# Kernel optimization log

Hardware: AMD Instinct MI355X
Metric: run time of the kernel (lower is better)

The kernel has to match this reference:

```python
import jax, jax.numpy as jnp
import numpy as np

B, IMG, TXT, N, FF, HID, C, E = 1024, 512, 300, 14, 2048, 128, 14, 182
D = IMG + TXT  # 812, transformer d_model


def setup_inputs() -> dict:
    key = jax.random.key(0)
    ks = jax.random.split(key, 12)
    r = lambda k, s, sc=0.02: (jax.random.normal(k, s, jnp.float32) * sc)
    return {
        "img_feat": jax.random.normal(ks[0], (B, IMG), jnp.float32),
        "word_embeds": jax.random.normal(ks[1], (N, TXT), jnp.float32),
        "edge_index": jax.random.randint(ks[2], (2, E), 0, N, jnp.int32),
        "in_proj_w": r(ks[3], (3 * D, D)),
        "in_proj_b": jnp.zeros((3 * D,), jnp.float32),
        "out_proj_w": r(ks[4], (D, D)),
        "out_proj_b": jnp.zeros((D,), jnp.float32),
        "ln1_g": jnp.ones((D,), jnp.float32), "ln1_b": jnp.zeros((D,), jnp.float32),
        "ln2_g": jnp.ones((D,), jnp.float32), "ln2_b": jnp.zeros((D,), jnp.float32),
        "ffn_w1": r(ks[5], (D, FF)), "ffn_b1": jnp.zeros((FF,), jnp.float32),
        "ffn_w2": r(ks[6], (FF, D)), "ffn_b2": jnp.zeros((D,), jnp.float32),
        "gcn1_w": r(ks[7], (D, HID)), "gcn1_b": jnp.zeros((HID,), jnp.float32),
        "gcn2_w": r(ks[8], (HID, HID)), "gcn2_b": jnp.zeros((HID,), jnp.float32),
        "lin_w": r(ks[9], (HID, C)), "lin_b": jnp.zeros((C,), jnp.float32),
    }


def layer_norm(x, g, b, eps=1e-5):
    mu = x.mean(-1, keepdims=True)
    var = ((x - mu) ** 2).mean(-1, keepdims=True)
    return (x - mu) * jax.lax.rsqrt(var + eps) * g + b


def gcn_conv(x, edge_index, W, b, n_nodes):
    # PyG GCNConv: add self loops, symmetric normalization, x @ W then scatter-add.
    # x: (B, N, F_in); gather/scatter along node axis (node_dim=-2).
    src, dst = edge_index[0], edge_index[1]
    loop = jnp.arange(n_nodes, dtype=src.dtype)
    src = jnp.concatenate([src, loop])
    dst = jnp.concatenate([dst, loop])
    deg = jnp.zeros((n_nodes,), x.dtype).at[dst].add(1.0)
    dinv = jnp.where(deg > 0, deg ** -0.5, 0.0)
    ew = dinv[src] * dinv[dst]                       # (E+N,)
    h = x @ W                                        # (B, N, F_out)
    msg = h[:, src, :] * ew[None, :, None]           # gather neighbors
    out = jnp.zeros_like(h).at[:, dst, :].add(msg)   # scatter-aggregate
    return out + b


def reference(img_feat, word_embeds, edge_index,
              in_proj_w, in_proj_b, out_proj_w, out_proj_b,
              ln1_g, ln1_b, ln2_g, ln2_b,
              ffn_w1, ffn_b1, ffn_w2, ffn_b2,
              gcn1_w, gcn1_b, gcn2_w, gcn2_b, lin_w, lin_b):
    # Broadcast image feature across the 14 label nodes; concat word embeddings.
    node = jnp.concatenate([
        jnp.broadcast_to(img_feat[:, None, :], (B, N, IMG)),
        jnp.broadcast_to(word_embeds[None, :, :], (B, N, TXT)),
    ], axis=-1)                                      # (B, N, D)

    # torch TransformerEncoderLayer, batch_first=False, nhead=1, post-norm, relu.
    # Input (B, N, D) is interpreted as (seq=B, batch=N, D): attention over dim 0.
    qkv = node @ in_proj_w.T + in_proj_b
    q, k, v = jnp.split(qkv, 3, axis=-1)             # each (B, N, D)
    scale = 1.0 / jnp.sqrt(jnp.asarray(D, node.dtype))
    scores = jnp.einsum('lnd,mnd->nlm', q, k) * scale  # (N, B, B)
    attn = jax.nn.softmax(scores, axis=-1)
    ao = jnp.einsum('nlm,mnd->lnd', attn, v)           # (B, N, D)
    ao = ao @ out_proj_w.T + out_proj_b
    x = layer_norm(node + ao, ln1_g, ln1_b)
    ff = jax.nn.relu(x @ ffn_w1 + ffn_b1) @ ffn_w2 + ffn_b2
    x = layer_norm(x + ff, ln2_g, ln2_b)               # (B, N, D)

    # Two GCNConv layers over the 14-node label graph (batched over B).
    x = jax.nn.relu(gcn_conv(x, edge_index, gcn1_w, gcn1_b, N))
    x = gcn_conv(x, edge_index, gcn2_w, gcn2_b, N)
    x = jax.nn.relu(x.mean(axis=1))                    # mean over nodes -> (B, HID)
    return x @ lin_w + lin_b                           # (B, C)
```

## Files before the change

### kernel.cpp

```cpp
#include <hip/hip_runtime.h>
#include <math.h>

#define B_    1024
#define IMG_  512
#define TXT_  300
#define NN_   14
#define FF_   2048
#define HID_  128
#define CC_   14
#define EE_   182
#define DD_   812
#define D3_   2436
#define BNR_  14336
#define KP_   832
#define TXP_  320
#define AROWS_ 1152

typedef __bf16 bf16x8 __attribute__((ext_vector_type(8)));
typedef float  f32x4  __attribute__((ext_vector_type(4)));
typedef unsigned short u16;

__device__ __forceinline__ u16 f2bf(float f) {
    union { float f; unsigned u; } v; v.f = f;
    unsigned r = v.u + 0x7FFFu + ((v.u >> 16) & 1u);
    return (u16)(r >> 16);
}
__device__ __forceinline__ float bf2f(u16 h) {
    union { unsigned u; float f; } v; v.u = ((unsigned)h) << 16; return v.f;
}

__device__ __forceinline__ void gload_lds16(const u16* g, u16* l) {
    __builtin_amdgcn_global_load_lds(
        (const __attribute__((address_space(1))) void*)g,
        (__attribute__((address_space(3))) void*)l, 16, 0, 0);
}

#define OFF_IMGB  0ULL
#define OFF_WIB   1048576ULL
#define OFF_WORDB 3543040ULL
#define OFF_WITX  3624960ULL
#define OFF_GB    0ULL
#define OFF_EBUF  29360128ULL
#define OFF_AVOT  33611776ULL
#define OFF_WOB   35446784ULL
#define OFF_HB    0ULL
#define OFF_PB    58720256ULL
#define OFF_X1B   82001920ULL
#define OFF_YB    105857024ULL
#define OFF_W1T   129712128ULL
#define OFF_W2T   133120000ULL
#define OFF_AQB   152420352ULL
#define OFF_TVB   158307552ULL
#define OFF_CO    158520544ULL
#define OFF_Z     158566016ULL
#define OFF_ADJ   158623360ULL
#define OFF_WG1T  158624384ULL
#define OFF_WG2T  158837376ULL

__device__ __forceinline__ void gemm_epi(
    float v, int rm, int cn, int epi,
    float* __restrict__ Cf, int ldc, u16* __restrict__ Cb, int ldcb,
    const float* __restrict__ bias)
{
    if (epi == 0) Cf[(size_t)rm * ldc + cn] = v;
    else if (epi == 1) { v += bias[cn]; v = v > 0.f ? v : 0.f;
                    Cb[(size_t)rm * ldcb + cn] = f2bf(v); }
    else if (epi == 2) Cf[(size_t)rm * ldc + cn] =
                    v + bias[cn] + bf2f(Cb[(size_t)rm * ldcb + cn]);
    else if (epi == 3) Cb[(size_t)rm * ldcb + cn] = f2bf(v);
    else if (epi == 4) { int bs = cn / DD_, cc = cn - bs * DD_;
                    Cb[(size_t)bs * (AROWS_ * KP_) + (size_t)rm * KP_ + cc] = f2bf(v); }
    else if (epi == 5) { float invz = 1.0f / bias[rm];
                    Cb[(size_t)rm * ldcb + cn] = f2bf(v * invz); }
    else if (epi == 6) Cf[(size_t)rm * ldc + cn] = v + bias[cn];
    else if (epi == 7) { const u16* rx = (const u16*)Cf;
                    Cb[(size_t)rm * ldcb + cn] =
                        f2bf(v + bias[cn] + bf2f(rx[(size_t)rm * ldc + cn])); }
    else if (epi == 8) {
        float t = v + bias[cn];
        if (cn < DD_) Cb[(size_t)(1024 + rm) * KP_ + cn] = f2bf(t);
        else if (cn >= 2 * DD_)
            ((u16*)Cf)[(size_t)rm * KP_ + (cn - 2 * DD_)] = f2bf(t);
    }
}

__device__ __forceinline__ void gemm_body4(
    const u16* __restrict__ A, int lda,
    const u16* __restrict__ Bm, int ldb,
    int M, int N, int K, float scale,
    float* __restrict__ Cf, int ldc,
    u16* __restrict__ Cb, int ldcb,
    const float* __restrict__ bias,
    int nxt, int swiz, int epi, int id)
{
    __shared__ __align__(16) u16 As[2][128 * 32];
    __shared__ __align__(16) u16 Bs[2][128 * 32];
    const int tid = threadIdx.x;
    int bx, by;
    if (swiz) { int r8 = id & 7; int q = id >> 3; bx = q % nxt; by = (q / nxt) * 8 + r8; }
    else      { bx = id % nxt; by = id / nxt; }
    const int row0 = by * 128, col0 = bx * 128;
    const int lane = tid & 63, wv = tid >> 6;
    const int wm = (wv >> 1) * 64, wn = (wv & 1) * 64;
    const int fr = lane & 15, qd = lane >> 4;

    const int s_r0  = (wv * 64 + lane) >> 2;
    const int s_ko  = (lane & 3) * 8;
    const int s_b0  = (wv * 64) * 8;
    const u16* Arow0 = A  + (size_t)(row0 + s_r0) * lda + s_ko;
    const u16* Arow1 = A  + (size_t)(row0 + s_r0 + 64) * lda + s_ko;
    const u16* Brow0 = Bm + (size_t)(col0 + s_r0) * ldb + s_ko;
    const u16* Brow1 = Bm + (size_t)(col0 + s_r0 + 64) * ldb + s_ko;

    f32x4 acc[4][4] = {};

    const int T = K >> 5;
    gload_lds16(Arow0, &As[0][s_b0]);
    gload_lds16(Arow1, &As[0][s_b0 + 2048]);
    gload_lds16(Brow0, &Bs[0][s_b0]);
    gload_lds16(Brow1, &Bs[0][s_b0 + 2048]);

    for (int i = 0; i < T; ++i) {
        __syncthreads();
        const int cur = i & 1;
        if (i + 1 < T) {
            const int nb = cur ^ 1;
            const int ko = (i + 1) << 5;
            gload_lds16(Arow0 + ko, &As[nb][s_b0]);
            gload_lds16(Arow1 + ko, &As[nb][s_b0 + 2048]);
            gload_lds16(Brow0 + ko, &Bs[nb][s_b0]);
            gload_lds16(Brow1 + ko, &Bs[nb][s_b0 + 2048]);
        }
        bf16x8 af[4], bg[4];
        #pragma unroll
        for (int j = 0; j < 4; ++j) {
            af[j] = *(const bf16x8*)&As[cur][(wm + j * 16 + fr) * 32 + qd * 8];
            bg[j] = *(const bf16x8*)&Bs[cur][(wn + j * 16 + fr) * 32 + qd * 8];
        }
        #pragma unroll
        for (int mi = 0; mi < 4; ++mi)
            #pragma unroll
            for (int ni = 0; ni < 4; ++ni)
                acc[mi][ni] = __builtin_amdgcn_mfma_f32_16x16x32_bf16(
                    af[mi], bg[ni], acc[mi][ni], 0, 0, 0);
    }

    #pragma unroll
    for (int mi = 0; mi < 4; ++mi) {
        #pragma unroll
        for (int i = 0; i < 4; ++i) {
            int rm = row0 + wm + mi * 16 + qd * 4 + i;
            if (rm >= M) continue;
            #pragma unroll
            for (int ni = 0; ni < 4; ++ni) {
                int cn = col0 + wn + ni * 16 + fr;
                if (cn >= N) continue;
                gemm_epi(acc[mi][ni][i] * scale, rm, cn, epi, Cf, ldc, Cb, ldcb, bias);
            }
        }
    }
}

__device__ __forceinline__ void gemm_body8(
    const u16* __restrict__ A, int lda,
    const u16* __restrict__ Bm, int ldb,
    int M, int N, int K, float scale,
    float* __restrict__ Cf, int ldc,
    u16* __restrict__ Cb, int ldcb,
    const float* __restrict__ bias,
    int nxt, int swiz, int epi, int id)
{
    __shared__ __align__(16) u16 As[2][128 * 32];
    __shared__ __align__(16) u16 Bs[2][128 * 32];
    const int tid = threadIdx.x;
    int bx, by;
    if (swiz) { int r8 = id & 7; int q = id >> 3; bx = q % nxt; by = (q / nxt) * 8 + r8; }
    else      { bx = id % nxt; by = id / nxt; }
    const int row0 = by * 128, col0 = bx * 128;
    const int lane = tid & 63, wv = tid >> 6;
    const int wm = (wv >> 1) * 32, wn = (wv & 1) * 64;
    const int fr = lane & 15, qd = lane >> 4;

    const int s_b0  = wv * 512;
    const int s_row = tid >> 2;
    const int s_ko  = (tid & 3) * 8;
    const u16* Arow = A  + (size_t)(row0 + s_row) * lda + s_ko;
    const u16* Brow = Bm + (size_t)(col0 + s_row) * ldb + s_ko;

    f32x4 acc[2][4] = {};

    const int T = K >> 5;
    gload_lds16(Arow, &As[0][s_b0]);
    gload_lds16(Brow, &Bs[0][s_b0]);

    for (int i = 0; i < T; ++i) {
        __syncthreads();
        const int cur = i & 1;
        if (i + 1 < T) {
            const int ko = (i + 1) << 5;
            gload_lds16(Arow + ko, &As[cur ^ 1][s_b0]);
            gload_lds16(Brow + ko, &Bs[cur ^ 1][s_b0]);
        }
        bf16x8 af[2], bg[4];
        #pragma unroll
        for (int j = 0; j < 2; ++j)
            af[j] = *(const bf16x8*)&As[cur][(wm + j * 16 + fr) * 32 + qd * 8];
        #pragma unroll
        for (int j = 0; j < 4; ++j)
            bg[j] = *(const bf16x8*)&Bs[cur][(wn + j * 16 + fr) * 32 + qd * 8];
        #pragma unroll
        for (int mi = 0; mi < 2; ++mi)
            #pragma unroll
            for (int ni = 0; ni < 4; ++ni)
                acc[mi][ni] = __builtin_amdgcn_mfma_f32_16x16x32_bf16(
                    af[mi], bg[ni], acc[mi][ni], 0, 0, 0);
    }

    #pragma unroll
    for (int mi = 0; mi < 2; ++mi) {
        #pragma unroll
        for (int i = 0; i < 4; ++i) {
            int rm = row0 + wm + mi * 16 + qd * 4 + i;
            if (rm >= M) continue;
            #pragma unroll
            for (int ni = 0; ni < 4; ++ni) {
                int cn = col0 + wn + ni * 16 + fr;
                if (cn >= N) continue;
                gemm_epi(acc[mi][ni][i] * scale, rm, cn, epi, Cf, ldc, Cb, ldcb, bias);
            }
        }
    }
}

template<int EPI>
__global__ __launch_bounds__(256, 4)
void bgemm(const u16* __restrict__ A, int lda,
           const u16* __restrict__ Bm, int ldb,
           int M, int N, int K, float scale,
           float* __restrict__ Cf, int ldc,
           u16* __restrict__ Cb, int ldcb,
           const float* __restrict__ bias,
           int nxt, int swiz)
{
    gemm_body4(A, lda, Bm, ldb, M, N, K, scale, Cf, ldc, Cb, ldcb, bias,
               nxt, swiz, EPI, blockIdx.x);
}

struct GDesc {
    const u16* A; const u16* B; float* Cf; u16* Cb; const float* bias;
    int lda, ldb, ldc, ldcb, M, N, K, epi, nxt, swiz, blk0;
    float scale;
};
struct TDesc { const float* src; u16* dst; int srs, drs, rows, cols, padrows, rt, nblk; };
struct MPack { GDesc g[3]; TDesc t[2]; const int* ei; float* Adj; int ng, gtot, nt; };

__device__ __forceinline__ void castT_body(TDesc T, int id)
{
    __shared__ float t[32][33];
    const int bx = id % T.rt, by = id / T.rt;
    const int r0 = bx * 32, c0 = by * 32;
    const int tx = threadIdx.x & 31, ty = threadIdx.x >> 5;
    #pragma unroll
    for (int k = 0; k < 2; ++k) {
        int r = r0 + ty + k * 16, c = c0 + tx;
        t[ty + k * 16][tx] = (r < T.rows && c < T.cols) ? T.src[(size_t)r * T.srs + c] : 0.f;
    }
    __syncthreads();
    #pragma unroll
    for (int k = 0; k < 2; ++k) {
        int c = c0 + ty + k * 16, r = r0 + tx;
        if (c < T.cols && r < T.padrows)
            T.dst[(size_t)c * T.drs + r] = f2bf(t[tx][ty + k * 16]);
    }
}

__device__ __forceinline__ void adj_body(const int* __restrict__ ei, float* __restrict__ Adj)
{
    __shared__ float degS[NN_], dinvS[NN_], adjS[NN_ * NN_];
    const int tid = threadIdx.x;
    if (tid < NN_) degS[tid] = 1.f;
    if (tid < NN_ * NN_) adjS[tid] = 0.f;
    __syncthreads();
    int s = 0, d = 0;
    if (tid < EE_) { s = ei[tid]; d = ei[EE_ + tid]; atomicAdd(&degS[d], 1.f); }
    __syncthreads();
    if (tid < NN_) dinvS[tid] = rsqrtf(degS[tid]);
    __syncthreads();
    if (tid < EE_) atomicAdd(&adjS[d * NN_ + s], dinvS[s] * dinvS[d]);
    if (tid < NN_) atomicAdd(&adjS[tid * NN_ + tid], dinvS[tid] * dinvS[tid]);
    __syncthreads();
    if (tid < NN_ * NN_) Adj[tid] = adjS[tid];
    if (tid < 16) {
        float sum = 0.f;
        if (tid < NN_)
            for (int j = 0; j < NN_; ++j) sum += adjS[j * NN_ + tid];
        Adj[NN_ * NN_ + tid] = sum / (float)NN_;
    }
}

__global__ __launch_bounds__(512, 6)
void kern_mix(MPack p)
{
    int id = blockIdx.x;
    if (id < p.gtot) {
        int si = 0;
        for (int s = 1; s < p.ng; ++s) if (id >= p.g[s].blk0) si = s;
        GDesc D = p.g[si];
        gemm_body8(D.A, D.lda, D.B, D.ldb, D.M, D.N, D.K, D.scale,
                   D.Cf, D.ldc, D.Cb, D.ldcb, D.bias, D.nxt, D.swiz, D.epi,
                   id - D.blk0);
        return;
    }
    id -= p.gtot;
    for (int s = 0; s < p.nt; ++s) {
        if (id < p.t[s].nblk) { castT_body(p.t[s], id); return; }
        id -= p.t[s].nblk;
    }
    if (id == 0 && p.ei) adj_body(p.ei, p.Adj);
}

struct CDesc { const float* src; u16* dst; int srs, drs, dcols, scols; };
struct CPack { CDesc d[9]; unsigned cum[10]; int n; };

__global__ void kern_mcast(CPack p)
{
    unsigned idx = blockIdx.x * 256 + threadIdx.x;
    int si = -1;
    for (int s = 0; s < p.n; ++s)
        if (idx >= p.cum[s] && idx < p.cum[s + 1]) { si = s; break; }
    if (si < 0) return;
    CDesc D = p.d[si];
    unsigned k = idx - p.cum[si];
    int r = k / D.dcols, c = k - r * D.dcols;
    D.dst[(size_t)r * D.drs + c] =
        (c < D.scols) ? f2bf(D.src[(size_t)r * D.srs + c]) : (u16)0;
}

__global__ __launch_bounds__(256) void kern_eG(const float* __restrict__ S,
    u16* __restrict__ Gb, float* __restrict__ Z)
{
    __shared__ float red[256];
    __shared__ u16 ews[NN_ * 1024];
    const int l = blockIdx.x, tid = threadIdx.x;
    const int lane = tid & 63, wv = tid >> 6;

    const float* wraw = S + 1024 * 1024;
    for (int z = wv; z < NN_; z += 4) {
        const float* r = wraw + z * 1024;
        float vv[16], mx = -1e30f;
        #pragma unroll
        for (int j = 0; j < 16; ++j) { vv[j] = r[lane + 64 * j]; mx = fmaxf(mx, vv[j]); }
        #pragma unroll
        for (int off = 32; off > 0; off >>= 1) mx = fmaxf(mx, __shfl_down(mx, off));
        mx = __shfl(mx, 0);
        #pragma unroll
        for (int j = 0; j < 16; ++j)
            ews[z * 1024 + lane + 64 * j] = f2bf(expf(vv[j] - mx));
    }
    const float* row = S + (size_t)l * 1024;
    float m = -1e30f;
    #pragma unroll
    for (int k = 0; k < 4; ++k) m = fmaxf(m, row[tid + 256 * k]);
    red[tid] = m; __syncthreads();
    for (int s = 128; s > 0; s >>= 1) {
        if (tid < s) red[tid] = fmaxf(red[tid], red[tid + s]);
        __syncthreads();
    }
    m = red[0];
    float ev[16];
    #pragma unroll
    for (int j = 0; j < 16; ++j) ev[j] = expf(row[lane + 64 * j] - m);
    u16* gr = Gb + (size_t)l * NN_ * 1024;
    for (int z = wv; z < NN_; z += 4) {
        const u16* er = &ews[z * 1024];
        float s = 0.f;
        #pragma unroll
        for (int j = 0; j < 16; ++j) {
            float pv = ev[j] * bf2f(er[lane + 64 * j]);
            gr[(size_t)z * 1024 + lane + 64 * j] = f2bf(pv);
            s += pv;
        }
        #pragma unroll
        for (int off = 32; off > 0; off >>= 1) s += __shfl_down(s, off);
        if (lane == 0) Z[l * NN_ + z] = s;
    }
}

__global__ __launch_bounds__(256) void kern_ln1(
    const float* __restrict__ img, const float* __restrict__ word,
    const u16* __restrict__ Pb,
    const float* __restrict__ co, const float* __restrict__ g,
    const float* __restrict__ bta, u16* __restrict__ Xb)
{
    __shared__ float buf[DD_];
    __shared__ float red[256];
    __shared__ float stats[2];
    int row = blockIdx.x;
    int b = row / NN_, n = row - b * NN_;
    const u16* pr = Pb + (size_t)row * DD_;
    const float* cr = co + n * DD_;
    float s = 0.f;
    for (int d = threadIdx.x; d < DD_; d += 256) {
        float v = (d < IMG_) ? img[(size_t)b * IMG_ + d] : word[n * TXT_ + d - IMG_];
        v += bf2f(pr[d]) + cr[d];
        buf[d] = v; s += v;
    }
    red[threadIdx.x] = s; __syncthreads();
    for (int t = 128; t > 0; t >>= 1) {
        if (threadIdx.x < t) red[threadIdx.x] += red[threadIdx.x + t];
        __syncthreads();
    }
    if (threadIdx.x == 0) stats[0] = red[0] / DD_;
    __syncthreads();
    float mu = stats[0], s2 = 0.f;
    for (int d = threadIdx.x; d < DD_; d += 256) { float t = buf[d] - mu; s2 += t * t; }
    red[threadIdx.x] = s2; __syncthreads();
    for (int t = 128; t > 0; t >>= 1) {
        if (threadIdx.x < t) red[threadIdx.x] += red[threadIdx.x + t];
        __syncthreads();
    }
    if (threadIdx.x == 0) stats[1] = rsqrtf(red[0] / DD_ + 1e-5f);
    __syncthreads();
    float rstd = stats[1];
    u16* xb = Xb + (size_t)row * KP_;
    for (int d = threadIdx.x; d < DD_; d += 256)
        xb[d] = f2bf((buf[d] - mu) * rstd * g[d] + bta[d]);
    for (int d = DD_ + threadIdx.x; d < KP_; d += 256) xb[d] = 0;
}

#define X2S_ 840
#define G1S_ 136
__global__ __launch_bounds__(256, 4)
void kern_gcn(const u16* __restrict__ Yb,
              const float* __restrict__ g2v, const float* __restrict__ bt2,
              const u16* __restrict__ Wg1T, const float* __restrict__ bg1,
              const u16* __restrict__ Wg2T, const float* __restrict__ bg2,
              const float* __restrict__ Wl,  const float* __restrict__ bl,
              const float* __restrict__ AdjW, float* __restrict__ out)
{
    __shared__ __align__(16) u16 x2s[16 * X2S_];
    __shared__ __align__(16) float h1s[16 * 132];
    __shared__ float adj_s[NN_ * NN_];
    __shared__ float colw_s[16];
    __shared__ float pool_s[HID_];
    u16* g1s = x2s;
    const int b = blockIdx.x, tid = threadIdx.x;
    const int lane = tid & 63, wv = tid >> 6;
    const int fr = lane & 15, qd = lane >> 4;

    if (tid < NN_ * NN_) adj_s[tid] = AdjW[tid];
    if (tid >= NN_ * NN_ && tid < NN_ * NN_ + 16) colw_s[tid - NN_ * NN_] = AdjW[tid];
    for (int k = tid; k < 2 * X2S_; k += 256) x2s[14 * X2S_ + k] = 0;
    for (int k = tid; k < 14 * (X2S_ - DD_); k += 256) {
        int j = k / (X2S_ - DD_), c = k - j * (X2S_ - DD_);
        x2s[j * X2S_ + DD_ + c] = 0;
    }

    for (int j = wv; j < NN_; j += 4) {
        const u16* yr = Yb + (size_t)(b * NN_ + j) * KP_;
        float vv[13], s = 0.f;
        #pragma unroll
        for (int k = 0; k < 13; ++k) {
            int d = lane + 64 * k;
            float v = (d < DD_) ? bf2f(yr[d]) : 0.f;
            vv[k] = v; s += v;
        }
        #pragma unroll
        for (int off = 32; off > 0; off >>= 1) s += __shfl_down(s, off);
        s = __shfl(s, 0);
        float mu = s / (float)DD_, s2 = 0.f;
        #pragma unroll
        for (int k = 0; k < 13; ++k) {
            int d = lane + 64 * k;
            float t = (d < DD_) ? vv[k] - mu : 0.f;
            s2 += t * t;
        }
        #pragma unroll
        for (int off = 32; off > 0; off >>= 1) s2 += __shfl_down(s2, off);
        s2 = __shfl(s2, 0);
        float rstd = rsqrtf(s2 / (float)DD_ + 1e-5f);
        #pragma unroll
        for (int k = 0; k < 13; ++k) {
            int d = lane + 64 * k;
            if (d < DD_)
                x2s[j * X2S_ + d] = f2bf((vv[k] - mu) * rstd * g2v[d] + bt2[d]);
        }
    }
    __syncthreads();

    {
        f32x4 acc[2] = {{}, {}};
        const u16* wp0 = Wg1T + (size_t)(wv * 32 + fr) * KP_ + qd * 8;
        const u16* wp1 = wp0 + (size_t)16 * KP_;
        bf16x8 bc0 = *(const bf16x8*)wp0;
        bf16x8 bc1 = *(const bf16x8*)wp1;
        for (int k0 = 0; k0 < KP_; k0 += 32) {
            bf16x8 bn0 = bc0, bn1 = bc1;
            if (k0 + 32 < KP_) {
                bn0 = *(const bf16x8*)(wp0 + k0 + 32);
                bn1 = *(const bf16x8*)(wp1 + k0 + 32);
            }
            bf16x8 af = *(const bf16x8*)&x2s[fr * X2S_ + k0 + qd * 8];
            acc[0] = __builtin_amdgcn_mfma_f32_16x16x32_bf16(af, bc0, acc[0], 0, 0, 0);
            acc[1] = __builtin_amdgcn_mfma_f32_16x16x32_bf16(af, bc1, acc[1], 0, 0, 0);
            bc0 = bn0; bc1 = bn1;
        }
        #pragma unroll
        for (int t = 0; t < 2; ++t)
            #pragma unroll
            for (int i = 0; i < 4; ++i)
                h1s[(qd * 4 + i) * 132 + wv * 32 + t * 16 + fr] = acc[t][i];
    }
    __syncthreads();

    {
        const int f = tid & 127, jj = (tid >> 7) * 7;
        #pragma unroll
        for (int j = 0; j < 7; ++j) {
            float s = bg1[f];
            #pragma unroll
            for (int i = 0; i < NN_; ++i)
                s = fmaf(adj_s[(jj + j) * NN_ + i], h1s[i * 132 + f], s);
            g1s[(jj + j) * G1S_ + f] = f2bf(s > 0.f ? s : 0.f);
        }
        for (int k = tid; k < 2 * G1S_; k += 256) g1s[14 * G1S_ + k] = 0;
    }
    __syncthreads();

    {
        f32x4 acc[2] = {{}, {}};
        const u16* wp0 = Wg2T + (size_t)(wv * 32 + fr) * HID_ + qd * 8;
        const u16* wp1 = wp0 + (size_t)16 * HID_;
        bf16x8 bc0 = *(const bf16x8*)wp0;
        bf16x8 bc1 = *(const bf16x8*)wp1;
        for (int k0 = 0; k0 < HID_; k0 += 32) {
            bf16x8 bn0 = bc0, bn1 = bc1;
            if (k0 + 32 < HID_) {
                bn0 = *(const bf16x8*)(wp0 + k0 + 32);
                bn1 = *(const bf16x8*)(wp1 + k0 + 32);
            }
            bf16x8 af = *(const bf16x8*)&g1s[fr * G1S_ + k0 + qd * 8];
            acc[0] = __builtin_amdgcn_mfma_f32_16x16x32_bf16(af, bc0, acc[0], 0, 0, 0);
            acc[1] = __builtin_amdgcn_mfma_f32_16x16x32_bf16(af, bc1, acc[1], 0, 0, 0);
            bc0 = bn0; bc1 = bn1;
        }
        #pragma unroll
        for (int t = 0; t < 2; ++t) {
            float s = 0.f;
            #pragma unroll
            for (int i = 0; i < 4; ++i) s += colw_s[qd * 4 + i] * acc[t][i];
            s += __shfl_xor(s, 16);
            s += __shfl_xor(s, 32);
            if (qd == 0) {
                int f = wv * 32 + t * 16 + fr;
                float p = s + bg2[f];
                pool_s[f] = p > 0.f ? p : 0.f;
            }
        }
    }
    __syncthreads();

    if (tid < CC_) {
        float s = bl[tid];
        #pragma unroll 8
        for (int f = 0; f < HID_; ++f)
            s = fmaf(pool_s[f], Wl[(size_t)f * CC_ + tid], s);
        out[(size_t)b * CC_ + tid] = s;
    }
}

extern "C" void kernel_launch(void* const* d_in, const int* in_sizes, int n_in,
                              void* d_out, int out_size, void* d_ws, size_t ws_size,
                              hipStream_t stream)
{
    const float* img  = (const float*)d_in[0];
    const float* word = (const float*)d_in[1];
    const int*   ei   = (const int*)d_in[2];
    const float* Wi   = (const float*)d_in[3];
    const float* bi   = (const float*)d_in[4];
    const float* Wo   = (const float*)d_in[5];
    const float* bo   = (const float*)d_in[6];
    const float* g1   = (const float*)d_in[7];
    const float* bt1  = (const float*)d_in[8];
    const float* g2   = (const float*)d_in[9];
    const float* bt2  = (const float*)d_in[10];
    const float* W1   = (const float*)d_in[11];
    const float* bf1  = (const float*)d_in[12];
    const float* W2   = (const float*)d_in[13];
    const float* bf2  = (const float*)d_in[14];
    const float* Wg1  = (const float*)d_in[15];
    const float* bg1  = (const float*)d_in[16];
    const float* Wg2  = (const float*)d_in[17];
    const float* bg2  = (const float*)d_in[18];
    const float* Wl   = (const float*)d_in[19];
    const float* bl   = (const float*)d_in[20];
    float* out = (float*)d_out;

    char* ws = (char*)d_ws;
    u16*   imgb = (u16*)  (ws + OFF_IMGB);
    u16*   Wib  = (u16*)  (ws + OFF_WIB);
    u16*   wordb= (u16*)  (ws + OFF_WORDB);
    u16*   WiTX = (u16*)  (ws + OFF_WITX);
    u16*   Gb   = (u16*)  (ws + OFF_GB);
    float* Ebuf = (float*)(ws + OFF_EBUF);
    u16*   AvoT = (u16*)  (ws + OFF_AVOT);
    u16*   Wob  = (u16*)  (ws + OFF_WOB);
    u16*   Hb   = (u16*)  (ws + OFF_HB);
    u16*   Pb   = (u16*)  (ws + OFF_PB);
    u16*   X1b  = (u16*)  (ws + OFF_X1B);
    u16*   Yb   = (u16*)  (ws + OFF_YB);
    u16*   W1T  = (u16*)  (ws + OFF_W1T);
    u16*   W2T  = (u16*)  (ws + OFF_W2T);
    u16*   Aqb  = (u16*)  (ws + OFF_AQB);
    u16*   Akb  = Aqb + AROWS_ * KP_;
    u16*   Avb  = Aqb + 2 * AROWS_ * KP_;
    u16*   Tvb  = (u16*)  (ws + OFF_TVB);
    float* co   = (float*)(ws + OFF_CO);
    float* Zb   = (float*)(ws + OFF_Z);
    float* Adj  = (float*)(ws + OFF_ADJ);
    u16*   Wg1T = (u16*)  (ws + OFF_WG1T);
    u16*   Wg2T = (u16*)  (ws + OFF_WG2T);

    const float scl = 1.0f / sqrtf((float)DD_);

    {
        CPack p; p.n = 9;
        unsigned c = 0;
        auto seg = [&](int i, const float* s, int srs, u16* d, int drs,
                       int rows, int dcols, int scols) {
            p.d[i] = { s, d, srs, drs, dcols, scols };
            p.cum[i] = c; c += (unsigned)rows * dcols;
        };
        seg(0, img,        IMG_, imgb,  IMG_, B_,   IMG_, IMG_);
        seg(1, Wi,         DD_,  Wib,   IMG_, D3_,  IMG_, IMG_);
        seg(2, word,       TXT_, wordb, TXP_, NN_,  TXP_, TXT_);
        seg(3, Wi + IMG_,  DD_,  WiTX,  TXP_, D3_,  TXP_, TXT_);
        seg(4, Wo,         DD_,  Wob,   KP_,  DD_,  KP_,  DD_);
        seg(5, nullptr, 0, Aqb + DD_,                    KP_, 1038, 20, 0);
        seg(6, nullptr, 0, Aqb + AROWS_ * KP_ + DD_,     KP_, 1024, 20, 0);
        seg(7, nullptr, 0, Aqb + 2 * AROWS_ * KP_ + DD_, KP_, 1024, 20, 0);
        seg(8, nullptr, 0, Tvb + DD_,                    KP_, NN_,  20, 0);
        p.cum[9] = c;
        kern_mcast<<<(c + 255) / 256, 256, 0, stream>>>(p);
    }

    {
        MPack p{};
        p.ng = 2; p.gtot = 180;
        p.g[0] = { wordb, WiTX, (float*)Tvb, Aqb, bi,
                   TXP_, TXP_, 0, 0, NN_, D3_, TXP_, 8, 20, 0, 0, 1.f };
        p.g[1] = { imgb, Wib, nullptr, Aqb, nullptr,
                   IMG_, IMG_, 0, 0, B_, D3_, IMG_, 4, 20, 1, 20, 1.f };
        p.nt = 2;
        p.t[0] = { Wg1, Wg1T, HID_, KP_,  DD_,  HID_, KP_,  26, 26 * 4 };
        p.t[1] = { Wg2, Wg2T, HID_, HID_, HID_, HID_, HID_, 4,  4 * 4 };
        p.ei = ei; p.Adj = Adj;
        kern_mix<<<180 + 104 + 16 + 1, 512, 0, stream>>>(p);
    }

    {
        MPack p{};
        p.ng = 3; p.gtot = 135;
        p.g[0] = { Aqb, Akb, Ebuf, nullptr, nullptr,
                   KP_, KP_, 1024, 0, 1024 + NN_, 1024, KP_, 0, 8, 0, 0, scl };
        p.g[1] = { Wob, Avb, nullptr, AvoT, nullptr,
                   KP_, KP_, 0, 1024, DD_, B_, KP_, 3, 8, 0, 72, 1.f };
        p.g[2] = { Tvb, Wob, co, nullptr, bo,
                   KP_, KP_, DD_, 0, NN_, DD_, KP_, 6, 7, 0, 128, 1.f };
        p.nt = 2;
        p.t[0] = { W1, W1T, FF_, KP_, DD_, FF_, KP_, 26, 26 * 64 };
        p.t[1] = { W2, W2T, DD_, FF_, FF_, DD_, FF_, 64, 64 * 26 };
        p.ei = nullptr; p.Adj = nullptr;
        kern_mix<<<135 + 1664 + 1664, 512, 0, stream>>>(p);
    }

    kern_eG<<<1024, 256, 0, stream>>>(Ebuf, Gb, Zb);

    bgemm<5><<<7 * 112, 256, 0, stream>>>(Gb, 1024, AvoT, 1024,
        BNR_, DD_, 1024, 1.f, nullptr, 0, Pb, DD_, Zb, 7, 1);

    kern_ln1<<<BNR_, 256, 0, stream>>>(img, word, Pb, co, g1, bt1, X1b);

    bgemm<1><<<16 * 112, 256, 0, stream>>>(X1b, KP_, W1T, KP_,
        BNR_, FF_, KP_, 1.f, nullptr, 0, Hb, FF_, bf1, 16, 1);
    bgemm<7><<<7 * 112, 256, 0, stream>>>(Hb, FF_, W2T, FF_,
        BNR_, DD_, FF_, 1.f, (float*)X1b, KP_, Yb, KP_, bf2, 7, 1);

    kern_gcn<<<B_, 256, 0, stream>>>(Yb, g2, bt2, Wg1T, bg1, Wg2T, bg2,
                                     Wl, bl, Adj, out);
}
```

Baseline: 455.0 us.

## Replace 128x128 GEMM with 256x256-tile, 4-stage pipelined, LDS-swizzled kernel

Swaps the three large transformer GEMMs to a new kernel with 256x256 output tiles, 512 threads and a 4-deep LDS ring buffer, fed by direct global-to-LDS loads with explicit vmcnt waits. LDS reads use an XOR swizzle to avoid bank conflicts. MFMA phases are split into two halves with barriers, s_setprio raises priority during the math, and block IDs are remapped across groups of eight. The goal is more data reuse per tile and better hiding of load latency. In exchange, 128KB of LDS allows only one block per CU, and the N=812 GEMMs now launch just 224 blocks, which may leave CUs idle and pads more wasted columns.

```diff
diff --git a/kernel.cpp b/kernel.cpp
--- a/kernel.cpp
+++ b/kernel.cpp
@@ -84,69 +84,117 @@
     }
 }
 
-__device__ __forceinline__ void gemm_body4(
+__device__ __forceinline__ void gemm256_body(
     const u16* __restrict__ A, int lda,
     const u16* __restrict__ Bm, int ldb,
     int M, int N, int K, float scale,
     float* __restrict__ Cf, int ldc,
     u16* __restrict__ Cb, int ldcb,
     const float* __restrict__ bias,
-    int nxt, int swiz, int epi, int id)
-{
-    __shared__ __align__(16) u16 As[2][128 * 32];
-    __shared__ __align__(16) u16 Bs[2][128 * 32];
+    int nxt, int epi, int id)
+{
+    __shared__ __align__(16) u16 As[4][8192];
+    __shared__ __align__(16) u16 Bs[4][8192];
     const int tid = threadIdx.x;
-    int bx, by;
-    if (swiz) { int r8 = id & 7; int q = id >> 3; bx = q % nxt; by = (q / nxt) * 8 + r8; }
-    else      { bx = id % nxt; by = id / nxt; }
-    const int row0 = by * 128, col0 = bx * 128;
+    const int bx = id % nxt, by = id / nxt;
+    const int row0 = by << 8, col0 = bx << 8;
     const int lane = tid & 63, wv = tid >> 6;
-    const int wm = (wv >> 1) * 64, wn = (wv & 1) * 64;
+    const int wm = (wv >> 2) << 7;
+    const int wn = (wv & 3) << 6;
     const int fr = lane & 15, qd = lane >> 4;
 
-    const int s_r0  = (wv * 64 + lane) >> 2;
-    const int s_ko  = (lane & 3) * 8;
-    const int s_b0  = (wv * 64) * 8;
-    const u16* Arow0 = A  + (size_t)(row0 + s_r0) * lda + s_ko;
-    const u16* Arow1 = A  + (size_t)(row0 + s_r0 + 64) * lda + s_ko;
-    const u16* Brow0 = Bm + (size_t)(col0 + s_r0) * ldb + s_ko;
-    const u16* Brow1 = Bm + (size_t)(col0 + s_r0 + 64) * ldb + s_ko;
-
-    f32x4 acc[4][4] = {};
-
+    int aoff[8], boff[4];
+    #pragma unroll
+    for (int mi = 0; mi < 8; ++mi) {
+        int r = wm + mi * 16 + fr;
+        aoff[mi] = r * 32 + ((qd ^ ((r >> 1) & 3)) << 3);
+    }
+    #pragma unroll
+    for (int ni = 0; ni < 4; ++ni) {
+        int r = wn + ni * 16 + fr;
+        boff[ni] = r * 32 + ((qd ^ ((r >> 1) & 3)) << 3);
+    }
+
+    const int i0 = tid, i1 = 512 + tid;
+    const int r0 = i0 >> 2, r1 = i1 >> 2;
+    const int c0 = ((i0 & 3) ^ ((r0 >> 1) & 3)) << 3;
+    const int c1 = ((i1 & 3) ^ ((r1 >> 1) & 3)) << 3;
+    const u16* Ag0 = A  + (size_t)(row0 + r0) * lda + c0;
+    const u16* Ag1 = A  + (size_t)(row0 + r1) * lda + c1;
+    const u16* Bg0 = Bm + (size_t)(col0 + r0) * ldb + c0;
+    const u16* Bg1 = Bm + (size_t)(col0 + r1) * ldb + c1;
+    const int lb0 = wv * 512;
+    const int lb1 = 4096 + wv * 512;
+
+    f32x4 acc[8][4] = {};
     const int T = K >> 5;
-    gload_lds16(Arow0, &As[0][s_b0]);
-    gload_lds16(Arow1, &As[0][s_b0 + 2048]);
-    gload_lds16(Brow0, &Bs[0][s_b0]);
-    gload_lds16(Brow1, &Bs[0][s_b0 + 2048]);
-
-    for (int i = 0; i < T; ++i) {
-        __syncthreads();
-        const int cur = i & 1;
-        if (i + 1 < T) {
-            const int nb = cur ^ 1;
-            const int ko = (i + 1) << 5;
-            gload_lds16(Arow0 + ko, &As[nb][s_b0]);
-            gload_lds16(Arow1 + ko, &As[nb][s_b0 + 2048]);
-            gload_lds16(Brow0 + ko, &Bs[nb][s_b0]);
-            gload_lds16(Brow1 + ko, &Bs[nb][s_b0 + 2048]);
-        }
-        bf16x8 af[4], bg[4];
-        #pragma unroll
-        for (int j = 0; j < 4; ++j) {
-            af[j] = *(const bf16x8*)&As[cur][(wm + j * 16 + fr) * 32 + qd * 8];
-            bg[j] = *(const bf16x8*)&Bs[cur][(wn + j * 16 + fr) * 32 + qd * 8];
-        }
-        #pragma unroll
-        for (int mi = 0; mi < 4; ++mi)
-            #pragma unroll
-            for (int ni = 0; ni < 4; ++ni)
-                acc[mi][ni] = __builtin_amdgcn_mfma_f32_16x16x32_bf16(
-                    af[mi], bg[ni], acc[mi][ni], 0, 0, 0);
-    }
-
-    #pragma unroll
-    for (int mi = 0; mi < 4; ++mi) {
+
+    #pragma unroll
+    for (int p = 0; p < 3; ++p) {
+        const int ko = p << 5;
+        gload_lds16(Ag0 + ko, &As[p][lb0]);
+        gload_lds16(Ag1 + ko, &As[p][lb1]);
+        gload_lds16(Bg0 + ko, &Bs[p][lb0]);
+        gload_lds16(Bg1 + ko, &Bs[p][lb1]);
+    }
+    asm volatile("s_waitcnt vmcnt(8)" ::: "memory");
+    __builtin_amdgcn_s_barrier();
+    __builtin_amdgcn_sched_barrier(0);
+
+    for (int t = 0; t < T; ++t) {
+        const int slot = t & 3;
+        const u16* as = &As[slot][0];
+        const u16* bs = &Bs[slot][0];
+        const int ns = (t + 3) & 3;
+        const int ko = (t + 3) << 5;
+        const bool pf = (t + 3 < T);
+
+        bf16x8 a[8];
+        #pragma unroll
+        for (int mi = 0; mi < 8; ++mi)
+            a[mi] = *(const bf16x8*)(as + aoff[mi]);
+        bf16x8 b0 = *(const bf16x8*)(bs + boff[0]);
+        bf16x8 b1 = *(const bf16x8*)(bs + boff[1]);
+        if (pf) {
+            gload_lds16(Ag0 + ko, &As[ns][lb0]);
+            gload_lds16(Ag1 + ko, &As[ns][lb1]);
+        }
+        __builtin_amdgcn_s_barrier();
+        __builtin_amdgcn_s_setprio(1);
+        #pragma unroll
+        for (int mi = 0; mi < 8; ++mi) {
+            acc[mi][0] = __builtin_amdgcn_mfma_f32_16x16x32_bf16(
+                a[mi], b0, acc[mi][0], 0, 0, 0);
+            acc[mi][1] = __builtin_amdgcn_mfma_f32_16x16x32_bf16(
+                a[mi], b1, acc[mi][1], 0, 0, 0);
+        }
+        __builtin_amdgcn_s_setprio(0);
+        __builtin_amdgcn_s_barrier();
+
+        bf16x8 b2 = *(const bf16x8*)(bs + boff[2]);
+        bf16x8 b3 = *(const bf16x8*)(bs + boff[3]);
+        if (pf) {
+            gload_lds16(Bg0 + ko, &Bs[ns][lb0]);
+            gload_lds16(Bg1 + ko, &Bs[ns][lb1]);
+        }
+        if (t < T - 3) asm volatile("s_waitcnt vmcnt(8)" ::: "memory");
+        else           asm volatile("s_waitcnt vmcnt(0)" ::: "memory");
+        __builtin_amdgcn_s_barrier();
+        __builtin_amdgcn_s_setprio(1);
+        #pragma unroll
+        for (int mi = 0; mi < 8; ++mi) {
+            acc[mi][2] = __builtin_amdgcn_mfma_f32_16x16x32_bf16(
+                a[mi], b2, acc[mi][2], 0, 0, 0);
+            acc[mi][3] = __builtin_amdgcn_mfma_f32_16x16x32_bf16(
+                a[mi], b3, acc[mi][3], 0, 0, 0);
+        }
+        __builtin_amdgcn_s_setprio(0);
+        __builtin_amdgcn_s_barrier();
+        __builtin_amdgcn_sched_barrier(0);
+    }
+
+    #pragma unroll
+    for (int mi = 0; mi < 8; ++mi) {
         #pragma unroll
         for (int i = 0; i < 4; ++i) {
             int rm = row0 + wm + mi * 16 + qd * 4 + i;
@@ -159,6 +207,23 @@
             }
         }
     }
+}
+
+template<int EPI>
+__global__ __launch_bounds__(512, 2)
+void bgemm256(const u16* __restrict__ A, int lda,
+              const u16* __restrict__ Bm, int ldb,
+              int M, int N, int K, float scale,
+              float* __restrict__ Cf, int ldc,
+              u16* __restrict__ Cb, int ldcb,
+              const float* __restrict__ bias,
+              int nxt)
+{
+    const int g8 = (int)gridDim.x >> 3;
+    const int id = (int)blockIdx.x;
+    const int w = (id & 7) * g8 + (id >> 3);
+    gemm256_body(A, lda, Bm, ldb, M, N, K, scale, Cf, ldc, Cb, ldcb, bias,
+                 nxt, EPI, w);
 }
 
 __device__ __forceinline__ void gemm_body8(
@@ -230,20 +295,6 @@
             }
         }
     }
-}
-
-template<int EPI>
-__global__ __launch_bounds__(256, 4)
-void bgemm(const u16* __restrict__ A, int lda,
-           const u16* __restrict__ Bm, int ldb,
-           int M, int N, int K, float scale,
-           float* __restrict__ Cf, int ldc,
-           u16* __restrict__ Cb, int ldcb,
-           const float* __restrict__ bias,
-           int nxt, int swiz)
-{
-    gemm_body4(A, lda, Bm, ldb, M, N, K, scale, Cf, ldc, Cb, ldcb, bias,
-               nxt, swiz, EPI, blockIdx.x);
 }
 
 struct GDesc {
@@ -676,15 +727,15 @@
 
     kern_eG<<<1024, 256, 0, stream>>>(Ebuf, Gb, Zb);
 
-    bgemm<5><<<7 * 112, 256, 0, stream>>>(Gb, 1024, AvoT, 1024,
-        BNR_, DD_, 1024, 1.f, nullptr, 0, Pb, DD_, Zb, 7, 1);
+    bgemm256<5><<<56 * 4, 512, 0, stream>>>(Gb, 1024, AvoT, 1024,
+        BNR_, DD_, 1024, 1.f, nullptr, 0, Pb, DD_, Zb, 4);
 
     kern_ln1<<<BNR_, 256, 0, stream>>>(img, word, Pb, co, g1, bt1, X1b);
 
-    bgemm<1><<<16 * 112, 256, 0, stream>>>(X1b, KP_, W1T, KP_,
-        BNR_, FF_, KP_, 1.f, nullptr, 0, Hb, FF_, bf1, 16, 1);
-    bgemm<7><<<7 * 112, 256, 0, stream>>>(Hb, FF_, W2T, FF_,
-        BNR_, DD_, FF_, 1.f, (float*)X1b, KP_, Yb, KP_, bf2, 7, 1);
+    bgemm256<1><<<56 * 8, 512, 0, stream>>>(X1b, KP_, W1T, KP_,
+        BNR_, FF_, KP_, 1.f, nullptr, 0, Hb, FF_, bf1, 8);
+    bgemm256<7><<<56 * 4, 512, 0, stream>>>(Hb, FF_, W2T, FF_,
+        BNR_, DD_, FF_, 1.f, (float*)X1b, KP_, Yb, KP_, bf2, 4);
 
     kern_gcn<<<B_, 256, 0, stream>>>(Yb, g2, bt2, Wg1T, bg1, Wg2T, bg2,
                                      Wl, bl, Adj, out);
```

Result: slower. 481.9 us (+5.9%).
